# Optimization experiments

Hardware: AMD Instinct MI355X
Metric: run time of the kernel (lower is better)

## Reference

```python
import jax, jax.numpy as jnp
import numpy as np

B, L, NC, D = 4, 2048, 4096, 128
ITERS = 4
NHEAD = 8
T = L // 2
C2 = 2 * D


def _ln(x, g, b, eps=1e-5):
    m = jnp.mean(x, axis=-1, keepdims=True)
    v = jnp.var(x, axis=-1, keepdims=True)
    return (x - m) * jax.lax.rsqrt(v + eps) * g + b


def _mlp3(x, W1, b1, W2, b2, W3, b3):
    h = jax.nn.relu(x @ W1 + b1)
    h = jax.nn.relu(h @ W2 + b2)
    return h @ W3 + b3


def _lstm(inp, h, c, Wih, Whh, gi, bi, gh, bh, gc, bc):
    gates = _ln(inp @ Wih, gi, bi) + _ln(h @ Whh, gh, bh)
    i, f, g, o = jnp.split(gates, 4, axis=-1)
    cy = _ln(jax.nn.sigmoid(f) * c + jax.nn.sigmoid(i) * jnp.tanh(g), gc, bc)
    hy = jax.nn.sigmoid(o) * jnp.tanh(cy)
    return hy, cy


def _flip(x):
    # flip matrix with full literal counts == permutation swapping pos/neg halves
    half = x.shape[1] // 2
    return jnp.concatenate([x[:, half:], x[:, :half]], axis=1)


def setup_inputs():
    key = jax.random.key(0)
    ks = iter(jax.random.split(key, 64))
    def xav(fi, fo):
        s = float(np.sqrt(6.0 / (fi + fo)))
        return jax.random.uniform(next(ks), (fi, fo), jnp.float32, -s, s)
    def rn(*shape):
        return jax.random.normal(next(ks), shape, jnp.float32)
    inp = {}
    inp['adjacency_matrices'] = (jax.random.uniform(next(ks), (B, L, NC)) < 0.03).astype(jnp.float32)
    inp['batch_lit_counts'] = jnp.full((B,), L, dtype=jnp.int32)
    inp['L_init'] = rn(1, D) / np.sqrt(D).astype(np.float32)
    inp['C_init'] = rn(1, D) / np.sqrt(D).astype(np.float32)
    for p in ('LC', 'CL'):
        for i in (1, 2, 3):
            inp[p + '_W' + str(i)] = xav(D, D)
            inp[p + '_b' + str(i)] = jnp.full((D,), 0.01, jnp.float32)
    for p, isz in (('Lu', 2 * D), ('Cu', D)):
        inp[p + '_Wih'] = rn(isz, 4 * D)  # torch uses raw randn for LSTM weights
        inp[p + '_Whh'] = rn(D, 4 * D)
        for ln, n in (('lni', 4 * D), ('lnh', 4 * D), ('lnc', D)):
            inp[p + '_' + ln + '_g'] = jnp.ones((n,), jnp.float32)
            inp[p + '_' + ln + '_b'] = jnp.zeros((n,), jnp.float32)
    for p in ('k', 'q', 'v'):
        inp['att_W' + p] = xav(C2, C2)
        inp['att_b' + p] = jnp.zeros((C2,), jnp.float32)
    for p in ('asn', 'vote'):
        inp[p + '_W1'] = xav(C2, D)
        inp[p + '_b1'] = jnp.full((D,), 0.01, jnp.float32)
        inp[p + '_W2'] = xav(D, 1)
        inp[p + '_b2'] = jnp.full((1,), 0.01, jnp.float32)
    return inp


def reference(adjacency_matrices, batch_lit_counts, L_init, C_init,
              LC_W1, LC_b1, LC_W2, LC_b2, LC_W3, LC_b3,
              CL_W1, CL_b1, CL_W2, CL_b2, CL_W3, CL_b3,
              Lu_Wih, Lu_Whh, Lu_lni_g, Lu_lni_b, Lu_lnh_g, Lu_lnh_b, Lu_lnc_g, Lu_lnc_b,
              Cu_Wih, Cu_Whh, Cu_lni_g, Cu_lni_b, Cu_lnh_g, Cu_lnh_b, Cu_lnc_g, Cu_lnc_b,
              att_Wk, att_bk, att_Wq, att_bq, att_Wv, att_bv,
              asn_W1, asn_b1, asn_W2, asn_b2, vote_W1, vote_b1, vote_W2, vote_b2):
    A = adjacency_matrices
    Bb, Ll, Cc = A.shape
    Lh = jnp.broadcast_to(L_init, (Bb, Ll, D))
    Lc = jnp.zeros_like(Lh)
    Ch = jnp.broadcast_to(C_init, (Bb, Cc, D))
    Cxc = jnp.zeros_like(Ch)
    for _ in range(ITERS):
        # literal -> clause messages (gather via A^T)
        LC = jnp.einsum('blc,bld->bcd', A, _mlp3(Lh, LC_W1, LC_b1, LC_W2, LC_b2, LC_W3, LC_b3))
        Ch, Cxc = _lstm(LC, Ch, Cxc, Cu_Wih, Cu_Whh, Cu_lni_g, Cu_lni_b, Cu_lnh_g, Cu_lnh_b, Cu_lnc_g, Cu_lnc_b)
        # clause -> literal messages (scatter via A)
        CL = jnp.einsum('blc,bcd->bld', A, _mlp3(Ch, CL_W1, CL_b1, CL_W2, CL_b2, CL_W3, CL_b3))
        Lh, Lc = _lstm(jnp.concatenate([CL, _flip(Lh)], axis=-1), Lh, Lc,
                       Lu_Wih, Lu_Whh, Lu_lni_g, Lu_lni_b, Lu_lnh_g, Lu_lnh_b, Lu_lnc_g, Lu_lnc_b)
    # readout [h_l ; h_{~l}], positive literals only
    read = jnp.concatenate([Lh, _flip(Lh)], axis=-1)[:, :T]  # [B,T,2D]
    half = batch_lit_counts // 2
    mask = (jnp.arange(T)[None, :] < half[:, None]).astype(read.dtype)  # [B,T]
    read = read * mask[:, :, None]
    hd = C2 // NHEAD
    def heads(x, W, b):
        return (x @ W + b).reshape(Bb, T, NHEAD, hd).transpose(0, 2, 1, 3)
    k = heads(read, att_Wk, att_bk)
    q = heads(read, att_Wq, att_bq)
    v = heads(read, att_Wv, att_bv)
    att = jnp.einsum('bhtd,bhsd->bhts', q, k) * (1.0 / np.sqrt(hd))
    sq = (mask[:, None, :, None] * mask[:, None, None, :]) > 0  # [B,1,T,T]
    att = jnp.where(sq, att, -jnp.inf)
    att = jax.nn.softmax(att, axis=-1)
    att = jnp.where(jnp.isnan(att), 0.0, att)
    y = jnp.einsum('bhts,bhsd->bhtd', att, v).transpose(0, 2, 1, 3).reshape(Bb, T, C2)
    def head_mlp(x, W1, b1, W2, b2):
        return jax.nn.sigmoid(jax.nn.relu(x @ W1 + b1) @ W2 + b2)[..., 0]
    assignments = head_mlp(y, asn_W1, asn_b1, asn_W2, asn_b2) * mask  # [B,T]
    vote_vals = head_mlp(y, vote_W1, vote_b1, vote_W2, vote_b2)
    votes = jnp.sum(vote_vals * mask, axis=1) / jnp.maximum(jnp.sum(mask, axis=1), 1.0)
    return votes, assignments
```

## Files before the change

### kernel.cpp

```cpp
#include <hip/hip_runtime.h>


#define B_    4
#define L_    2048
#define NC_   4096
#define D_    128
#define ITERS_ 4
#define NH_   8
#define T_    1024
#define C2_   256
#define HD_   32
#define BL_   (B_*L_)
#define BNC_  (B_*NC_)
#define QS_   768

typedef unsigned short u16;
typedef __attribute__((ext_vector_type(8))) short b16x8;
typedef __attribute__((ext_vector_type(4))) float f32x4;

static __device__ __forceinline__ float bf2f(u16 u){
  union{unsigned int i; float f;} x; x.i = ((unsigned int)u) << 16; return x.f;
}
static __device__ __forceinline__ u16 f2bf(float f){
  union{float f; unsigned int i;} x; x.f = f;
// ... 41 lines not shown

#define NPJ_ 16
struct PJobs { const void* src[NPJ_]; unsigned n[NPJ_], N[NPJ_], koff[NPJ_],
               ksb[NPJ_], dh[NPJ_], dl[NPJ_]; };

__global__ __launch_bounds__(256) void k_prep(PJobs pj, u16* __restrict__ up,
                                              const int* __restrict__ flag){
  int jj = blockIdx.y;
  unsigned n = pj.n[jj];
  unsigned g = blockIdx.x*256 + threadIdx.x;
  if (g >= n) return;
  unsigned j = g & 7, lane = (g>>3)&63;
  unsigned ksb = pj.ksb[jj];
  unsigned ks = (g>>9) & ((1u<<ksb)-1u);
  unsigned nt = g >> (9+ksb);
  unsigned ncol = nt*16 + (lane&15);
  unsigned k = pj.koff[jj] + ks*32 + ((lane>>4)&3)*8 + j;
  unsigned si = k*pj.N[jj] + ncol;
  float v;
  if (*flag) v = bf2f(((const u16*)pj.src[jj])[si]);
  else       v = ((const float*)pj.src[jj])[si];
  u16 h,l; split2(v, h, l);
  up[pj.dh[jj] + g] = h;
  up[pj.dl[jj] + g] = l;
}

__global__ __launch_bounds__(256) void k_init(float* __restrict__ h, float* __restrict__ c,
                                              const float* __restrict__ init, int n){
  int i = blockIdx.x*256 + threadIdx.x;
  if (i < n){ h[i] = init[i & (D_-1)]; c[i] = 0.f; }
}

__global__ void k_zero_u(unsigned* __restrict__ p, int n){
  int i = blockIdx.x*256 + threadIdx.x; if (i < n) p[i] = 0u;
}
__global__ void k_zero(float* p, int n){
  int i = blockIdx.x*64 + threadIdx.x; if (i < n) p[i] = 0.f;
}

__global__ __launch_bounds__(128) void k_pack(const void* __restrict__ A,
    unsigned* __restrict__ bits, unsigned* __restrict__ cnt_l,
    const int* __restrict__ flag){
  const int row = blockIdx.x, w = threadIdx.x;
  unsigned m = 0;
  if (*flag){
    const ushort4* p = (const ushort4*)A + (size_t)row*(NC_/4) + w*8;
    #pragma unroll
    for (int i = 0; i < 8; i++){
      ushort4 u = p[i];
      m |= (unsigned)(u.x != 0) << (i*4);
      m |= (unsigned)(u.y != 0) << (i*4+1);
      m |= (unsigned)(u.z != 0) << (i*4+2);
      m |= (unsigned)(u.w != 0) << (i*4+3);
    }
  } else {
    const float4* p = (const float4*)A + (size_t)row*(NC_/4) + w*8;
    #pragma unroll
    for (int i = 0; i < 8; i++){
      float4 v = p[i];
      m |= (unsigned)(v.x != 0.f) << (i*4);
      m |= (unsigned)(v.y != 0.f) << (i*4+1);
      m |= (unsigned)(v.z != 0.f) << (i*4+2);
      m |= (unsigned)(v.w != 0.f) << (i*4+3);
    }
  }
  bits[(size_t)row*128 + w] = m;
  unsigned pc = __popc(m);
  #pragma unroll
  for (int o = 1; o < 64; o <<= 1) pc += __shfl_xor(pc, o);
  __shared__ unsigned ss[2];
  if ((w & 63) == 0) ss[w >> 6] = pc;
  __syncthreads();
  if (w == 0) cnt_l[row] = ss[0] + ss[1];
}

__global__ __launch_bounds__(256) void k_scan(unsigned* __restrict__ cnt,
    unsigned* __restrict__ off, int n){
  __shared__ unsigned ps[257];
  int t = threadIdx.x;
  int seg = n >> 8;
  int base = t*seg;
  unsigned s = 0;
  for (int i = 0; i < seg; i++) s += cnt[base+i];
  ps[t] = s;
  __syncthreads();
  if (t == 0){
    unsigned run = 0;
    for (int i = 0; i < 256; i++){ unsigned x = ps[i]; ps[i] = run; run += x; }
    ps[256] = run;
  }
  __syncthreads();
  unsigned run = ps[t];
  for (int i = 0; i < seg; i++){ off[base+i] = run; run += cnt[base+i]; cnt[base+i] = 0u; }
  if (t == 0) off[n] = ps[256];
}

__global__ __launch_bounds__(128) void k_fill_l(const unsigned* __restrict__ bits,
    const unsigned* __restrict__ off_l, u16* __restrict__ val_l,
    unsigned* __restrict__ cnt_c){
  const int row = blockIdx.x, w = threadIdx.x;
  const int b = row >> 11;
  unsigned m = bits[(size_t)row*128 + w];
  unsigned pc = __popc(m);
  __shared__ unsigned s[128];
  s[w] = pc; __syncthreads();
  #pragma unroll
  for (int o = 1; o < 128; o <<= 1){
    unsigned v = (w >= o) ? s[w-o] : 0u;
    __syncthreads();
    s[w] += v;
    __syncthreads();
  }
  unsigned base = off_l[row] + s[w] - pc;
  unsigned cb = ((unsigned)b << 12) + w*32;
  while (m){
    int j = __ffs(m) - 1; m &= m - 1;
    val_l[base++] = (u16)(w*32 + j);
    atomicAdd(cnt_c + cb + j, 1u);
  }
}

__global__ __launch_bounds__(256) void k_fill_c(const unsigned* __restrict__ bits,
    const unsigned* __restrict__ off_c, unsigned* __restrict__ cur_c,
    u16* __restrict__ val_c){
  int g = blockIdx.x*256 + threadIdx.x;
  unsigned m = bits[g];
  int row = g >> 7, w = g & 127;
  int b = row >> 11, l = row & (L_-1);
  unsigned cb = ((unsigned)b << 12) + w*32;
  while (m){
    int j = __ffs(m) - 1; m &= m - 1;
    unsigned idx = cb + j;
    unsigned pos = atomicAdd(cur_c + idx, 1u);
    val_c[off_c[idx] + pos] = (u16)l;
  }
}

__global__ __launch_bounds__(256) void k_spmm(const unsigned* __restrict__ off,
    const u16* __restrict__ val, const float* __restrict__ M, float* __restrict__ out,
    int sh1, int sh2){
  int row  = blockIdx.x*4 + (threadIdx.x >> 6);
  int lane = threadIdx.x & 63;
  unsigned p0 = off[row], p1 = off[row+1];
  const float2* Mp = (const float2*)M + (((size_t)(row >> sh1) << sh2) * 64) + lane;
  float x = 0.f, y = 0.f;
  for (unsigned p = p0; p < p1; ++p){
    float2 v = Mp[(size_t)val[p] * 64];
    x += v.x; y += v.y;
  }
  float2 r; r.x = x; r.y = y;
  ((float2*)out)[(size_t)row*64 + lane] = r;
}

__global__ __launch_bounds__(512) void k_mlp3m(const float* __restrict__ X,
    const u16* __restrict__ W1h, const u16* __restrict__ W1l,
    const u16* __restrict__ W2h, const u16* __restrict__ W2l,
    const u16* __restrict__ W3h, const u16* __restrict__ W3l,
    const float* __restrict__ b1, const float* __restrict__ b2,
    const float* __restrict__ b3, float* __restrict__ Y)
{
  __shared__ __align__(16) u16 Ah[32*136];
  __shared__ __align__(16) u16 Al[32*136];
  const int tid = threadIdx.x, lane = tid & 63, wv = tid >> 6;
  const int quad = lane >> 4, l15 = lane & 15;
  const int r0 = blockIdx.x * 32;
  {
    int row = tid >> 4, c0 = (tid & 15)*8;
    const float4* src = (const float4*)(X + (size_t)(r0+row)*128 + c0);
    float4 v0 = src[0], v1 = src[1];
    u16 h,l;
    split2(v0.x,h,l); Ah[row*136+c0]  =h; Al[row*136+c0]  =l;
    split2(v0.y,h,l); Ah[row*136+c0+1]=h; Al[row*136+c0+1]=l;
    split2(v0.z,h,l); Ah[row*136+c0+2]=h; Al[row*136+c0+2]=l;
    split2(v0.w,h,l); Ah[row*136+c0+3]=h; Al[row*136+c0+3]=l;
    split2(v1.x,h,l); Ah[row*136+c0+4]=h; Al[row*136+c0+4]=l;
    split2(v1.y,h,l); Ah[row*136+c0+5]=h; Al[row*136+c0+5]=l;
    split2(v1.z,h,l); Ah[row*136+c0+6]=h; Al[row*136+c0+6]=l;
    split2(v1.w,h,l); Ah[row*136+c0+7]=h; Al[row*136+c0+7]=l;
  }
  __syncthreads();
  const u16* Whs[3] = {W1h, W2h, W3h};
  const u16* Wls[3] = {W1l, W2l, W3l};
  const float* bs[3] = {b1, b2, b3};
  #pragma unroll
  for (int layer = 0; layer < 3; layer++){
    f32x4 acc[2] = {};
    #pragma unroll
    for (int ks = 0; ks < 4; ks++){
      b16x8 a_h[2], a_l[2];
      #pragma unroll
      for (int mt = 0; mt < 2; mt++){
        int ao = (mt*16 + l15)*136 + ks*32 + quad*8;
        a_h[mt] = *(const b16x8*)(Ah + ao);
        a_l[mt] = *(const b16x8*)(Al + ao);
      }
      size_t bo = (size_t)((wv*4 + ks)*64 + lane)*8;
      b16x8 bh = *(const b16x8*)(Whs[layer] + bo);
      b16x8 bl = *(const b16x8*)(Wls[layer] + bo);
      #pragma unroll
      for (int mt = 0; mt < 2; mt++){
        acc[mt] = __builtin_amdgcn_mfma_f32_16x16x32_bf16(a_h[mt], bh, acc[mt],0,0,0);
        acc[mt] = __builtin_amdgcn_mfma_f32_16x16x32_bf16(a_h[mt], bl, acc[mt],0,0,0);
        acc[mt] = __builtin_amdgcn_mfma_f32_16x16x32_bf16(a_l[mt], bh, acc[mt],0,0,0);
      }
    }
    int col = wv*16 + l15;
    if (layer < 2){
      float bb = bs[layer][col];
      __syncthreads();
      #pragma unroll
      for (int mt = 0; mt < 2; mt++)
        #pragma unroll
        for (int r = 0; r < 4; r++){
          int row = mt*16 + quad*4 + r;
          float v = fmaxf(acc[mt][r] + bb, 0.f);
          u16 h,l; split2(v,h,l);
          Ah[row*136 + col] = h; Al[row*136 + col] = l;
        }
      __syncthreads();
    } else {
      float bb = bs[2][col];
      #pragma unroll
      for (int mt = 0; mt < 2; mt++)
        #pragma unroll
        for (int r = 0; r < 4; r++){
          int row = mt*16 + quad*4 + r;
          Y[(size_t)(r0+row)*128 + col] = acc[mt][r] + bb;
        }
    }
  }
}

template<int NSEG>
__global__ __launch_bounds__(512) void k_lstm_mfma(
    const float* __restrict__ A0, const float* __restrict__ A1, const float* __restrict__ A2,
    int flip1,
    const u16* __restrict__ W0h, const u16* __restrict__ W0l,
    const u16* __restrict__ W1h, const u16* __restrict__ W1l,
    const u16* __restrict__ W2h, const u16* __restrict__ W2l,
    const float* __restrict__ lni_g, const float* __restrict__ lni_b,
    const float* __restrict__ lnh_g, const float* __restrict__ lnh_b,
    const float* __restrict__ lnc_g, const float* __restrict__ lnc_b,
    const float* __restrict__ c_in, float* __restrict__ c_out,
    float* __restrict__ h_out)
{
  __shared__ __align__(16) float G[32*516];
  __shared__ float red[8][32][4];
  __shared__ float st[32][4];
  u16* Ah = (u16*)G;
  u16* Al = Ah + 32*136;
  const int tid = threadIdx.x, lane = tid & 63, wv = tid >> 6;
  const int quad = lane >> 4, l15 = lane & 15;
  const int r0 = blockIdx.x * 32;

  f32x4 acc1[2][4] = {}, acc2[2][4] = {};

  #pragma unroll
  for (int s = 0; s < NSEG; ++s){
    const float* Ap = (s==0) ? A0 : ((s==1) ? A1 : A2);
    const u16* Wh = (s==0) ? W0h : ((s==1) ? W1h : W2h);
    const u16* Wl = (s==0) ? W0l : ((s==1) ? W1l : W2l);
    const int fm = (s==1) ? flip1 : 0;
    __syncthreads();
    {
      int row = tid >> 4, c0 = (tid & 15)*8;
      int arow = (r0 + row) ^ fm;
      const float4* src = (const float4*)(Ap + (size_t)arow*128 + c0);
      float4 v0 = src[0], v1 = src[1];
      u16 h,l;
      split2(v0.x,h,l); Ah[row*136+c0]  =h; Al[row*136+c0]  =l;
      split2(v0.y,h,l); Ah[row*136+c0+1]=h; Al[row*136+c0+1]=l;
      split2(v0.z,h,l); Ah[row*136+c0+2]=h; Al[row*136+c0+2]=l;
      split2(v0.w,h,l); Ah[row*136+c0+3]=h; Al[row*136+c0+3]=l;
      split2(v1.x,h,l); Ah[row*136+c0+4]=h; Al[row*136+c0+4]=l;
      split2(v1.y,h,l); Ah[row*136+c0+5]=h; Al[row*136+c0+5]=l;
      split2(v1.z,h,l); Ah[row*136+c0+6]=h; Al[row*136+c0+6]=l;
      split2(v1.w,h,l); Ah[row*136+c0+7]=h; Al[row*136+c0+7]=l;
    }
    __syncthreads();
    f32x4 (*accp)[4] = (s == NSEG-1) ? acc2 : acc1;
    #pragma unroll
    for (int ks = 0; ks < 4; ks++){
      b16x8 a_h[2], a_l[2];
      #pragma unroll
      for (int mt = 0; mt < 2; mt++){
        int ao = (mt*16 + l15)*136 + ks*32 + quad*8;
        a_h[mt] = *(const b16x8*)(Ah + ao);
        a_l[mt] = *(const b16x8*)(Al + ao);
      }
      #pragma unroll
      for (int ntl = 0; ntl < 4; ntl++){
        int nt = wv*4 + ntl;
        size_t bo = (size_t)((nt*4 + ks)*64 + lane)*8;
        b16x8 bh = *(const b16x8*)(Wh + bo);
        b16x8 bl = *(const b16x8*)(Wl + bo);
        #pragma unroll
        for (int mt = 0; mt < 2; mt++){
          accp[mt][ntl] = __builtin_amdgcn_mfma_f32_16x16x32_bf16(a_h[mt], bh, accp[mt][ntl],0,0,0);
          accp[mt][ntl] = __builtin_amdgcn_mfma_f32_16x16x32_bf16(a_h[mt], bl, accp[mt][ntl],0,0,0);
          accp[mt][ntl] = __builtin_amdgcn_mfma_f32_16x16x32_bf16(a_l[mt], bh, accp[mt][ntl],0,0,0);
        }
      }
    }
  }

  #pragma unroll
  for (int mt = 0; mt < 2; mt++)
    #pragma unroll
    for (int r = 0; r < 4; r++){
      float s1=0.f, q1=0.f, s2=0.f, q2=0.f;
      #pragma unroll
      for (int ntl = 0; ntl < 4; ntl++){
        float v1 = acc1[mt][ntl][r]; s1 += v1; q1 += v1*v1;
        float v2 = acc2[mt][ntl][r]; s2 += v2; q2 += v2*v2;
      }
      #pragma unroll
      for (int m = 1; m < 16; m <<= 1){
        s1 += __shfl_xor(s1, m); q1 += __shfl_xor(q1, m);
        s2 += __shfl_xor(s2, m); q2 += __shfl_xor(q2, m);
      }
      if (l15 == 0){
        int row = mt*16 + quad*4 + r;
        red[wv][row][0]=s1; red[wv][row][1]=q1; red[wv][row][2]=s2; red[wv][row][3]=q2;
      }
    }
  __syncthreads();
  if (tid < 32){
    int row = tid;
    float s1=0.f,q1=0.f,s2=0.f,q2=0.f;
    #pragma unroll
    for (int w = 0; w < 8; w++){
      s1 += red[w][row][0]; q1 += red[w][row][1];
      s2 += red[w][row][2]; q2 += red[w][row][3];
    }
    const float i512 = 1.f/512.f;
    float m1 = s1*i512, v1 = fmaxf(q1*i512 - m1*m1, 0.f);
    float m2 = s2*i512, v2 = fmaxf(q2*i512 - m2*m2, 0.f);
    st[row][0] = m1; st[row][1] = rsqrtf(v1 + 1e-5f);
    st[row][2] = m2; st[row][3] = rsqrtf(v2 + 1e-5f);
  }
  __syncthreads();

  #pragma unroll
  for (int mt = 0; mt < 2; mt++)
    #pragma unroll
    for (int ntl = 0; ntl < 4; ntl++){
      int col = wv*64 + ntl*16 + l15;
      float gi = lni_g[col], bi = lni_b[col];
      float gh = lnh_g[col], bh = lnh_b[col];
      #pragma unroll
      for (int r = 0; r < 4; r++){
        int row = mt*16 + quad*4 + r;
        float v = (acc1[mt][ntl][r] - st[row][0])*st[row][1]*gi + bi
                + (acc2[mt][ntl][r] - st[row][2])*st[row][3]*gh + bh;
        G[row*516 + col] = v;
      }
    }
  __syncthreads();

  float lcg0 = lnc_g[lane], lcb0 = lnc_b[lane];
  float lcg1 = lnc_g[lane+64], lcb1 = lnc_b[lane+64];
  const float i128 = 1.f/128.f;
  #pragma unroll
  for (int i = 0; i < 4; i++){
    int row = wv*4 + i;
    int rg = r0 + row;
    float cp[2], sc = 0.f, qc = 0.f;
    #pragma unroll
    for (int jj = 0; jj < 2; jj++){
      int c = lane + 64*jj;
      float iv = sigm(G[row*516 + c]);
      float fv = sigm(G[row*516 + 128 + c]);
      float gv = tanhf(G[row*516 + 256 + c]);
      cp[jj] = fv * c_in[(size_t)rg*128 + c] + iv*gv;
      sc += cp[jj]; qc += cp[jj]*cp[jj];
    }
    #pragma unroll
    for (int m = 1; m < 64; m <<= 1){ sc += __shfl_xor(sc, m); qc += __shfl_xor(qc, m); }
    float mc = sc*i128, vc = fmaxf(qc*i128 - mc*mc, 0.f), rsc = rsqrtf(vc + 1e-5f);
    #pragma unroll
    for (int jj = 0; jj < 2; jj++){
      int c = lane + 64*jj;
      float cy = (cp[jj]-mc)*rsc*(jj ? lcg1 : lcg0) + (jj ? lcb1 : lcb0);
      c_out[(size_t)rg*128 + c] = cy;
      float ov = sigm(G[row*516 + 384 + c]);
      h_out[(size_t)rg*128 + c] = ov*tanhf(cy);
    }
  }
}

template<int NT, int NSPLIT, int KK32, int ACT, int GATHER>
__global__ __launch_bounds__(512) void k_gemm_mfma(const float* __restrict__ A,
    const u16* __restrict__ Wh, const u16* __restrict__ Wl,
    const float* __restrict__ bias, float* __restrict__ Y,
    const int* __restrict__ counts)
{
  const int NTOT = NSPLIT*8*NT*16;
  const int LDA = KK32*32 + 8;
  __shared__ __align__(16) u16 Ah[32*(KK32*32+8)];
  __shared__ __align__(16) u16 Al[32*(KK32*32+8)];
  const int tid = threadIdx.x, lane = tid & 63, wv = tid >> 6;
  const int quad = lane >> 4, l15 = lane & 15;
  const int r0 = blockIdx.x * 32, by = blockIdx.y;
  {
    int row = tid >> 4, c0 = (tid & 15)*(KK32*2);
    if (GATHER){
      int r = r0 + row; int b = r >> 10; int t = r & 1023;
      int half = counts[b] / 2; if (half > T_) half = T_;
      float msk = (t < half) ? 1.f : 0.f;
      #pragma unroll
      for (int q4 = 0; q4 < KK32/2; q4++){
        int c = c0 + q4*4;
        const float* src = A + ((size_t)(b*L_ + t + ((c >= 128) ? T_ : 0))*128 + (c & 127));
        float4 v = *(const float4*)src;
        u16 h,l;
        split2(v.x*msk,h,l); Ah[row*LDA+c]  =h; Al[row*LDA+c]  =l;
        split2(v.y*msk,h,l); Ah[row*LDA+c+1]=h; Al[row*LDA+c+1]=l;
        split2(v.z*msk,h,l); Ah[row*LDA+c+2]=h; Al[row*LDA+c+2]=l;
        split2(v.w*msk,h,l); Ah[row*LDA+c+3]=h; Al[row*LDA+c+3]=l;
      }
    } else {
      const float4* src = (const float4*)(A + (size_t)(r0+row)*(KK32*32) + c0);
      #pragma unroll
      for (int q4 = 0; q4 < KK32/2; q4++){
        float4 v = src[q4]; int c = c0 + q4*4;
        u16 h,l;
        split2(v.x,h,l); Ah[row*LDA+c]  =h; Al[row*LDA+c]  =l;
        split2(v.y,h,l); Ah[row*LDA+c+1]=h; Al[row*LDA+c+1]=l;
        split2(v.z,h,l); Ah[row*LDA+c+2]=h; Al[row*LDA+c+2]=l;
        split2(v.w,h,l); Ah[row*LDA+c+3]=h; Al[row*LDA+c+3]=l;
      }
    }
  }
  __syncthreads();
  f32x4 acc[2][NT] = {};
  #pragma unroll
  for (int ks = 0; ks < KK32; ks++){
    b16x8 a_h[2], a_l[2];
    #pragma unroll
    for (int mt = 0; mt < 2; mt++){
      int ao = (mt*16 + l15)*LDA + ks*32 + quad*8;
      a_h[mt] = *(const b16x8*)(Ah + ao);
      a_l[mt] = *(const b16x8*)(Al + ao);
    }
    #pragma unroll
    for (int ntl = 0; ntl < NT; ntl++){
      int nt = by*(8*NT) + wv*NT + ntl;
      size_t bo = (size_t)((nt*KK32 + ks)*64 + lane)*8;
      b16x8 bh = *(const b16x8*)(Wh + bo);
      b16x8 bl = *(const b16x8*)(Wl + bo);
      #pragma unroll
      for (int mt = 0; mt < 2; mt++){
        acc[mt][ntl] = __builtin_amdgcn_mfma_f32_16x16x32_bf16(a_h[mt], bh, acc[mt][ntl],0,0,0);
        acc[mt][ntl] = __builtin_amdgcn_mfma_f32_16x16x32_bf16(a_h[mt], bl, acc[mt][ntl],0,0,0);
        acc[mt][ntl] = __builtin_amdgcn_mfma_f32_16x16x32_bf16(a_l[mt], bh, acc[mt][ntl],0,0,0);
      }
    }
  }
  #pragma unroll
  for (int mt = 0; mt < 2; mt++)
    #pragma unroll
    for (int ntl = 0; ntl < NT; ntl++){
      int colg = by*(8*NT*16) + wv*(NT*16) + ntl*16 + l15;
      float bb = bias[colg];
      #pragma unroll
      for (int r = 0; r < 4; r++){
        int row = mt*16 + quad*4 + r;
        float v = acc[mt][ntl][r] + bb;
        if (ACT) v = fmaxf(v, 0.f);
        Y[(size_t)(r0+row)*NTOT + colg] = v;
      }
    }
}

__global__ __launch_bounds__(256) void k_attn_split(const float* __restrict__ qkv,
    const int* __restrict__ counts, float* __restrict__ Pa, float* __restrict__ ML)
{
  const int z = blockIdx.z, b = z >> 1, part = z & 1;
  const int h = blockIdx.y, t0 = blockIdx.x*64;
  int half = counts[b] / 2; if (half > T_) half = T_; if (half < 0) half = 0;
  const int sbeg = part*512;
  const int send = (half < sbeg + 512) ? half : (sbeg + 512);
  if (t0 >= half || sbeg >= send) return;
  const int tid = threadIdx.x;
  const int lane = tid & 63, wv = tid >> 6;
  const int lr = tid >> 2, lc = (tid & 3)*8;

  __shared__ float Qs[64][36];
  __shared__ float Ks[64][32];
  __shared__ float Ss[64][68];

  {
    const float* qp = qkv + (size_t)(b*T_ + t0 + lr)*QS_ + h*HD_ + lc;
    float4 a0 = *(const float4*)qp;
    float4 a1 = *(const float4*)(qp+4);
    *(float4*)&Qs[lr][lc]   = a0;
    *(float4*)&Qs[lr][lc+4] = a1;
  }

  const int ty = tid >> 4, tx = tid & 15;
  const int sr = wv*16 + (lane & 15);
  const int spart = (lane >> 4) * 16;
  const int rp = lane >> 3, cq = lane & 7;
  const int r0 = wv*16 + rp*2;

  float4 acc0 = {0.f,0.f,0.f,0.f}, acc1 = {0.f,0.f,0.f,0.f};
  float mst = -3e38f, lst = 0.f;
  const float scale = 0.17677669529663687f;
  const int ntile = (send - sbeg + 63) >> 6;

  for (int st = 0; st < ntile; ++st){
    const int s0 = sbeg + st*64;
    __syncthreads();
    {
      const float* kp = qkv + (size_t)(b*T_ + s0 + lr)*QS_ + 256 + h*HD_ + lc;
      float4 k0 = *(const float4*)kp;
      float4 k1 = *(const float4*)(kp+4);
      int key = (lr >> 2) & 7;
      int c0 = lc >> 2;
      *(float4*)&Ks[lr][4*((c0  ) ^ key)] = k0;
      *(float4*)&Ks[lr][4*((c0+1) ^ key)] = k1;
    }
    __syncthreads();

    float s4[4][4];
    #pragma unroll
    for (int i = 0; i < 4; i++)
      #pragma unroll
      for (int j = 0; j < 4; j++) s4[i][j] = 0.f;
    const int xk = tx & 7;
    #pragma unroll
    for (int kk4 = 0; kk4 < 8; kk4++){
      float4 a4[4], b4[4];
      #pragma unroll
      for (int i = 0; i < 4; i++) a4[i] = *(const float4*)&Qs[ty*4+i][kk4*4];
      const int pk = 4*(kk4 ^ xk);
      #pragma unroll
      for (int j = 0; j < 4; j++) b4[j] = *(const float4*)&Ks[tx*4+j][pk];
      #pragma unroll
      for (int i = 0; i < 4; i++)
        #pragma unroll
        for (int j = 0; j < 4; j++)
          s4[i][j] += a4[i].x*b4[j].x + a4[i].y*b4[j].y + a4[i].z*b4[j].z + a4[i].w*b4[j].w;
    }
    #pragma unroll
    for (int i = 0; i < 4; i++){
      float4 w4;
      w4.x = (s0 + tx*4 + 0 < half) ? s4[i][0]*scale : -1e30f;
      w4.y = (s0 + tx*4 + 1 < half) ? s4[i][1]*scale : -1e30f;
      w4.z = (s0 + tx*4 + 2 < half) ? s4[i][2]*scale : -1e30f;
      w4.w = (s0 + tx*4 + 3 < half) ? s4[i][3]*scale : -1e30f;
      *(float4*)&Ss[ty*4+i][tx*4] = w4;
    }

    float pvv[16];
    float vmax = -3e38f;
    #pragma unroll
    for (int c4 = 0; c4 < 4; c4++){
      float4 t4 = *(const float4*)&Ss[sr][spart + c4*4];
      pvv[c4*4+0] = t4.x; pvv[c4*4+1] = t4.y; pvv[c4*4+2] = t4.z; pvv[c4*4+3] = t4.w;
      vmax = fmaxf(vmax, fmaxf(fmaxf(t4.x, t4.y), fmaxf(t4.z, t4.w)));
    }
    vmax = fmaxf(vmax, __shfl_xor(vmax, 16));
    vmax = fmaxf(vmax, __shfl_xor(vmax, 32));
    float nm = fmaxf(mst, vmax);
    float alpha = expf(mst - nm);
    float psum = 0.f;
    #pragma unroll
    for (int c = 0; c < 16; c++){
      float p = expf(pvv[c] - nm);
      pvv[c] = p; psum += p;
    }
    psum += __shfl_xor(psum, 16);
    psum += __shfl_xor(psum, 32);
    lst = lst*alpha + psum;
    mst = nm;
    #pragma unroll
    for (int c4 = 0; c4 < 4; c4++){
      float4 w4; w4.x = pvv[c4*4+0]; w4.y = pvv[c4*4+1]; w4.z = pvv[c4*4+2]; w4.w = pvv[c4*4+3];
      *(float4*)&Ss[sr][spart + c4*4] = w4;
    }
    float al0 = __shfl(alpha, 2*rp);
    float al1 = __shfl(alpha, 2*rp + 1);
    acc0.x *= al0; acc0.y *= al0; acc0.z *= al0; acc0.w *= al0;
    acc1.x *= al1; acc1.y *= al1; acc1.z *= al1; acc1.w *= al1;

    const float* vbase = qkv + (size_t)(b*T_ + s0)*QS_ + 512 + h*HD_ + cq*4;
    #pragma unroll 4
    for (int kk4 = 0; kk4 < 16; kk4++){
      float4 p0 = *(const float4*)&Ss[r0  ][kk4*4];
      float4 p1 = *(const float4*)&Ss[r0+1][kk4*4];
      float4 v0 = *(const float4*)(vbase + (size_t)(kk4*4+0)*QS_);
      float4 v1 = *(const float4*)(vbase + (size_t)(kk4*4+1)*QS_);
      float4 v2 = *(const float4*)(vbase + (size_t)(kk4*4+2)*QS_);
      float4 v3 = *(const float4*)(vbase + (size_t)(kk4*4+3)*QS_);
      acc0.x += p0.x*v0.x + p0.y*v1.x + p0.z*v2.x + p0.w*v3.x;
      acc0.y += p0.x*v0.y + p0.y*v1.y + p0.z*v2.y + p0.w*v3.y;
      acc0.z += p0.x*v0.z + p0.y*v1.z + p0.z*v2.z + p0.w*v3.z;
      acc0.w += p0.x*v0.w + p0.y*v1.w + p0.z*v2.w + p0.w*v3.w;
      acc1.x += p1.x*v0.x + p1.y*v1.x + p1.z*v2.x + p1.w*v3.x;
      acc1.y += p1.x*v0.y + p1.y*v1.y + p1.z*v2.y + p1.w*v3.y;
      acc1.z += p1.x*v0.z + p1.y*v1.z + p1.z*v2.z + p1.w*v3.z;
      acc1.w += p1.x*v0.w + p1.y*v1.w + p1.z*v2.w + p1.w*v3.w;
    }
  }

  const int prow0 = (b*NH_ + h)*T_ + t0;
  float* accP = Pa + (size_t)part*1048576;
  *(float4*)(accP + (size_t)(prow0 + r0    )*32 + cq*4) = acc0;
  *(float4*)(accP + (size_t)(prow0 + r0 + 1)*32 + cq*4) = acc1;
  if (lane < 16){
    float* mlP = ML + (size_t)part*65536;
    int rr = prow0 + wv*16 + lane;
    mlP[(size_t)rr*2]   = mst;
    mlP[(size_t)rr*2+1] = lst;
  }
}

__global__ __launch_bounds__(256) void k_attn_comb(const float* __restrict__ Pa,
    const float* __restrict__ ML, const int* __restrict__ counts,
    float* __restrict__ y)
{
  int g = blockIdx.x*256 + threadIdx.x;
  int r = g >> 8, c = g & 255;
  int b = r >> 10, t = r & 1023;
  int h = c >> 5, cc = c & 31;
  int half = counts[b] / 2; if (half > T_) half = T_;
  float out = 0.f;
  if (t < half){
    int prow = (b*NH_ + h)*T_ + t;
    float m0 = ML[(size_t)prow*2], l0 = ML[(size_t)prow*2+1];
    float a0 = Pa[(size_t)prow*32 + cc];
    if (half > 512){
      float m1 = ML[65536 + (size_t)prow*2], l1 = ML[65536 + (size_t)prow*2+1];
      float a1 = Pa[1048576 + (size_t)prow*32 + cc];
      float m = fmaxf(m0, m1);
      float w0 = expf(m0 - m), w1 = expf(m1 - m);
      float den = w0*l0 + w1*l1;
      out = (den > 0.f) ? (w0*a0 + w1*a1)/den : 0.f;
    } else {
      out = (l0 > 0.f) ? a0/l0 : 0.f;
    }
  }
  y[(size_t)r*256 + c] = out;
}

__global__ __launch_bounds__(128) void k_final(const float* __restrict__ hv,
    const float* __restrict__ aW2, const float* __restrict__ ab2,
    const float* __restrict__ vW2, const float* __restrict__ vb2,
    const int* __restrict__ counts, void* __restrict__ outv,
    float* __restrict__ vote_sum, const int* __restrict__ flag)
{
  int row = blockIdx.x, tid = threadIdx.x;
  int b = row / T_, t = row - b*T_;
  int half = counts[b] / 2; if (half > T_) half = T_;
  float pa = hv[(size_t)row*256 + tid]       * aW2[tid];
  float pv = hv[(size_t)row*256 + 128 + tid] * vW2[tid];
  #pragma unroll
  for (int off = 32; off > 0; off >>= 1){ pa += __shfl_down(pa, off); pv += __shfl_down(pv, off); }
  __shared__ float r[2][2];
  int wid = tid >> 6, lane = tid & 63;
  if (lane == 0){ r[0][wid] = pa; r[1][wid] = pv; }
  __syncthreads();
  if (tid == 0){
    float a  = sigm(r[0][0] + r[0][1] + ab2[0]);
    float vv = sigm(r[1][0] + r[1][1] + vb2[0]);
    bool mk = (t < half);
    float av = mk ? a : 0.f;
    if (*flag) ((u16*)outv)[4 + row] = f2bf(av);
    else       ((float*)outv)[4 + row] = av;
    if (mk) atomicAdd(vote_sum + b, vv);
  }
}

__global__ void k_votes(const float* __restrict__ vote_sum, const int* __restrict__ counts,
                        void* __restrict__ outv, const int* __restrict__ flag){
  int b = threadIdx.x;
  if (b < B_){
    int half = counts[b] / 2; if (half > T_) half = T_;
    float den = (float)(half > 1 ? half : 1);
    float vv = vote_sum[b] / den;
    if (*flag) ((u16*)outv)[b] = f2bf(vv);
    else       ((float*)outv)[b] = vv;
  }
}

extern "C" void kernel_launch(void* const* d_in, const int* in_sizes, int n_in,
                              void* d_out, int out_size, void* d_ws, size_t ws_size,
                              hipStream_t stream)
{
  const void* A_adj = d_in[0];
  const int* counts = (const int*)d_in[1];

  const size_t M1 = (size_t)1048576;
  const size_t NEED = (5*M1 + M1 + 2*M1 + 2*M1 + 700416 + 16416 + 8224
                       + 16384 + 8192 + 520000 + 520000 + 32) * sizeof(float);
  if (ws_size < NEED) return;

  float* ws = (float*)d_ws;
  float* R    = ws;
  float* Lc   = R + 5*M1;
  float* Ch   = Lc + M1;
  float* Cc   = Ch + 2*M1;
  float* wp   = Cc + 2*M1;
  unsigned* off_c = (unsigned*)(wp + 700416);
  unsigned* off_l = off_c + 16416;
  unsigned* cnt_c = off_l + 8224;
  unsigned* cnt_l = cnt_c + 16384;
  u16* val_c = (u16*)(cnt_l + 8192);
  u16* val_l = (u16*)((float*)val_c + 520000);
  float* tail = (float*)val_l + 520000;
  float* vote_sum = tail;
  int* flag = (int*)(tail + 8);
  unsigned* bits = (unsigned*)R;

  float* R0 = R, *R1 = R + M1, *R2 = R + 2*M1, *R3 = R + 3*M1, *R4 = R + 4*M1;

  k_detect<<<1, 256, 0, stream>>>((const unsigned int*)A_adj, flag);

  CJobs cj;
  int ncj = 0;
  unsigned off = 0;
  auto cadd = [&](int idx, unsigned n)->float*{
    cj.src[ncj] = d_in[idx]; cj.n[ncj] = n; cj.off[ncj] = off;
    float* p = wp + off; off += (n + 3u) & ~3u; ncj++; return p;
  };
  float* Linit = cadd(2, 128);
  float* Cinit = cadd(3, 128);
  float *LC_b1 = cadd(5, 128), *LC_b2 = cadd(7, 128), *LC_b3 = cadd(9, 128);
  float *CL_b1 = cadd(11,128), *CL_b2 = cadd(13,128), *CL_b3 = cadd(15,128);
  float *Lu_lni_g = cadd(18,512), *Lu_lni_b = cadd(19,512);
  float *Lu_lnh_g = cadd(20,512), *Lu_lnh_b = cadd(21,512);
  float *Lu_lnc_g = cadd(22,128), *Lu_lnc_b = cadd(23,128);
  float *Cu_lni_g = cadd(26,512), *Cu_lni_b = cadd(27,512);
  float *Cu_lnh_g = cadd(28,512), *Cu_lnh_b = cadd(29,512);
  float *Cu_lnc_g = cadd(30,128), *Cu_lnc_b = cadd(31,128);
  float *asn_W2 = cadd(40,128), *asn_b2 = cadd(41,1);
  float *vote_W2 = cadd(44,128), *vote_b2 = cadd(45,1);
  float* bqkv = wp + off;
  cj.src[ncj]=d_in[35]; cj.n[ncj]=256; cj.off[ncj]=off;       ncj++;
  cj.src[ncj]=d_in[33]; cj.n[ncj]=256; cj.off[ncj]=off+256;   ncj++;
  cj.src[ncj]=d_in[37]; cj.n[ncj]=256; cj.off[ncj]=off+512;   ncj++;
  off += 768;
  float* bhv = wp + off;
  cj.src[ncj]=d_in[39]; cj.n[ncj]=128; cj.off[ncj]=off;       ncj++;
  cj.src[ncj]=d_in[43]; cj.n[ncj]=128; cj.off[ncj]=off+128;   ncj++;
  off += 256;
  { dim3 g(2, NCJ_); k_cvt_all<<<g, 256, 0, stream>>>(cj, wp, flag); }

  u16* up = (u16*)(wp + ((off + 3u) & ~3u));
  PJobs pj;
  int npj = 0;
  unsigned uoff = 0;
  auto padd = [&](int idx, unsigned n, unsigned Nw, unsigned koff, unsigned ksb,
                  unsigned dsth, unsigned dstl){
    pj.src[npj]=d_in[idx]; pj.n[npj]=n; pj.N[npj]=Nw; pj.koff[npj]=koff;
    pj.ksb[npj]=ksb; pj.dh[npj]=dsth; pj.dl[npj]=dstl; npj++;
  };
  auto solo = [&](int idx, unsigned n, unsigned Nw, unsigned koff, unsigned ksb,
                  const u16** h, const u16** l){
    padd(idx, n, Nw, koff, ksb, uoff, uoff + n);
    *h = up + uoff; *l = up + uoff + n; uoff += 2*n;
  };
  const u16 *lc1h,*lc1l,*lc2h,*lc2l,*lc3h,*lc3l,*cl1h,*cl1l,*cl2h,*cl2l,*cl3h,*cl3l;
  const u16 *cwih_h,*cwih_l,*cwhh_h,*cwhh_l;
  const u16 *lwa_h,*lwa_l,*lwb_h,*lwb_l,*lwhh_h,*lwhh_l;
  solo(4, 16384,128,0,2,&lc1h,&lc1l);  solo(6, 16384,128,0,2,&lc2h,&lc2l);
  solo(8, 16384,128,0,2,&lc3h,&lc3l);  solo(10,16384,128,0,2,&cl1h,&cl1l);
  solo(12,16384,128,0,2,&cl2h,&cl2l);  solo(14,16384,128,0,2,&cl3h,&cl3l);
  solo(24,65536,512,0,2,&cwih_h,&cwih_l);
  solo(25,65536,512,0,2,&cwhh_h,&cwhh_l);
  solo(16,65536,512,0,  2,&lwa_h,&lwa_l);
  solo(16,65536,512,128,2,&lwb_h,&lwb_l);
  solo(17,65536,512,0,2,&lwhh_h,&lwhh_l);
  const u16* wqkv_h = up + uoff;
  const u16* wqkv_l = up + uoff + 196608;
  padd(34, 65536, 256, 0, 3, uoff,           uoff+196608);
  padd(32, 65536, 256, 0, 3, uoff+65536,     uoff+196608+65536);
  padd(36, 65536, 256, 0, 3, uoff+131072,    uoff+196608+131072);
  uoff += 393216;
  const u16* whv_h = up + uoff;
  const u16* whv_l = up + uoff + 65536;
  padd(38, 32768, 128, 0, 3, uoff,        uoff+65536);
  padd(42, 32768, 128, 0, 3, uoff+32768,  uoff+65536+32768);
  uoff += 131072;
  { dim3 g(256, NPJ_); k_prep<<<g, 256, 0, stream>>>(pj, up, flag); }

  k_zero_u<<<(16384+255)/256, 256, 0, stream>>>(cnt_c, 16384);
  k_pack<<<BL_, 128, 0, stream>>>(A_adj, bits, cnt_l, flag);
  k_scan<<<1, 256, 0, stream>>>(cnt_l, off_l, 8192);
  k_fill_l<<<BL_, 128, 0, stream>>>(bits, off_l, val_l, cnt_c);
  k_scan<<<1, 256, 0, stream>>>(cnt_c, off_c, 16384);
  k_fill_c<<<4096, 256, 0, stream>>>(bits, off_c, cnt_c, val_c);

  k_init<<<(BL_*D_)/256, 256, 0, stream>>>(R0, Lc, Linit, BL_*D_);
  k_init<<<(BNC_*D_)/256, 256, 0, stream>>>(Ch, Cc, Cinit, BNC_*D_);

  for (int it = 0; it < ITERS_; ++it){
    bool ev = ((it & 1) == 0);
    float* cur  = ev ? R0 : R4;
    float* msgL = ev ? R1 : R0;
    float* LCb  = ev ? R2 : R1;
    float* msgC = LCb;
    float* CLb  = ev ? R1 : R3;
    float* nxt  = ev ? R4 : R0;

    k_mlp3m<<<BL_/32, 512, 0, stream>>>(cur, lc1h,lc1l, lc2h,lc2l, lc3h,lc3l,
                                        LC_b1, LC_b2, LC_b3, msgL);
    k_spmm<<<BNC_/4, 256, 0, stream>>>(off_c, val_c, msgL, LCb, 12, 11);
    k_lstm_mfma<2><<<BNC_/32, 512, 0, stream>>>(LCb, Ch, nullptr, 0,
        cwih_h, cwih_l, cwhh_h, cwhh_l, nullptr, nullptr,
        Cu_lni_g, Cu_lni_b, Cu_lnh_g, Cu_lnh_b, Cu_lnc_g, Cu_lnc_b, Cc, Cc, Ch);
    k_mlp3m<<<BNC_/32, 512, 0, stream>>>(Ch, cl1h,cl1l, cl2h,cl2l, cl3h,cl3l,
                                         CL_b1, CL_b2, CL_b3, msgC);
    k_spmm<<<BL_/4, 256, 0, stream>>>(off_l, val_l, msgC, CLb, 11, 12);
    k_lstm_mfma<3><<<BL_/32, 512, 0, stream>>>(CLb, cur, cur, 1024,
        lwa_h, lwa_l, lwb_h, lwb_l, lwhh_h, lwhh_l,
        Lu_lni_g, Lu_lni_b, Lu_lnh_g, Lu_lnh_b, Lu_lnc_g, Lu_lnc_b, Lc, Lc, nxt);
  }
  float* Lh = R0;

  float* qkvb  = Ch;
  float* yb    = R1;
  float* hv    = R2;

  { dim3 g((B_*T_)/32, 2);
    k_gemm_mfma<3,2,8,0,1><<<g, 512, 0, stream>>>(Lh, wqkv_h, wqkv_l, bqkv, qkvb, counts); }
  { dim3 g(T_/64, NH_, B_*2);
    k_attn_split<<<g, 256, 0, stream>>>(qkvb, counts, R3, Lc); }
  k_attn_comb<<<4096, 256, 0, stream>>>(R3, Lc, counts, yb);
  { dim3 g((B_*T_)/32, 2);
    k_gemm_mfma<1,2,8,1,0><<<g, 512, 0, stream>>>(yb, whv_h, whv_l, bhv, hv, counts); }
  k_zero<<<1, 64, 0, stream>>>(vote_sum, B_);
  k_final<<<B_*T_, 128, 0, stream>>>(hv, asn_W2, asn_b2, vote_W2, vote_b2,
                                     counts, d_out, vote_sum, flag);
  k_votes<<<1, 64, 0, stream>>>(vote_sum, counts, d_out, flag);
}
```

Baseline: 1.692 ms.

## Shrink MFMA GEMM row tiles to 16 rows with 256-thread blocks

The MLP, LSTM and generic GEMM kernels move from 32-row tiles with 8 waves to 16-row tiles with 4 waves. Each wave now covers twice as many output column tiles from a single A fragment, and the grids double in size. Launch bounds now request 4 blocks per CU, which may raise occupancy and shrink LDS per block. The cost is that each weight fragment is reused across only one row tile, so global weight traffic per row doubles, and register pressure per wave rises. The attention PV loop unroll is also lowered.

```diff
diff --git a/kernel.cpp b/kernel.cpp
--- a/kernel.cpp
+++ b/kernel.cpp
@@ -217,18 +217,18 @@
   ((float2*)out)[(size_t)row*64 + lane] = r;
 }
 
-__global__ __launch_bounds__(512) void k_mlp3m(const float* __restrict__ X,
+__global__ __launch_bounds__(256, 4) void k_mlp3m(const float* __restrict__ X,
     const u16* __restrict__ W1h, const u16* __restrict__ W1l,
     const u16* __restrict__ W2h, const u16* __restrict__ W2l,
     const u16* __restrict__ W3h, const u16* __restrict__ W3l,
     const float* __restrict__ b1, const float* __restrict__ b2,
     const float* __restrict__ b3, float* __restrict__ Y)
 {
-  __shared__ __align__(16) u16 Ah[32*136];
-  __shared__ __align__(16) u16 Al[32*136];
+  __shared__ __align__(16) u16 Ah[16*136];
+  __shared__ __align__(16) u16 Al[16*136];
   const int tid = threadIdx.x, lane = tid & 63, wv = tid >> 6;
   const int quad = lane >> 4, l15 = lane & 15;
-  const int r0 = blockIdx.x * 32;
+  const int r0 = blockIdx.x * 16;
   {
     int row = tid >> 4, c0 = (tid & 15)*8;
     const float4* src = (const float4*)(X + (size_t)(r0+row)*128 + c0);
@@ -252,52 +252,52 @@
     f32x4 acc[2] = {};
     #pragma unroll
     for (int ks = 0; ks < 4; ks++){
-      b16x8 a_h[2], a_l[2];
-      #pragma unroll
-      for (int mt = 0; mt < 2; mt++){
-        int ao = (mt*16 + l15)*136 + ks*32 + quad*8;
-        a_h[mt] = *(const b16x8*)(Ah + ao);
-        a_l[mt] = *(const b16x8*)(Al + ao);
+      int ao = l15*136 + ks*32 + quad*8;
+      b16x8 a_h = *(const b16x8*)(Ah + ao);
+      b16x8 a_l = *(const b16x8*)(Al + ao);
+      #pragma unroll
+      for (int ntl = 0; ntl < 2; ntl++){
+        int nt = wv*2 + ntl;
+        size_t bo = (size_t)((nt*4 + ks)*64 + lane)*8;
+        b16x8 bh = *(const b16x8*)(Whs[layer] + bo);
+        b16x8 bl = *(const b16x8*)(Wls[layer] + bo);
+        acc[ntl] = __builtin_amdgcn_mfma_f32_16x16x32_bf16(a_h, bh, acc[ntl],0,0,0);
+        acc[ntl] = __builtin_amdgcn_mfma_f32_16x16x32_bf16(a_h, bl, acc[ntl],0,0,0);
+        acc[ntl] = __builtin_amdgcn_mfma_f32_16x16x32_bf16(a_l, bh, acc[ntl],0,0,0);
       }
-      size_t bo = (size_t)((wv*4 + ks)*64 + lane)*8;
-      b16x8 bh = *(const b16x8*)(Whs[layer] + bo);
-      b16x8 bl = *(const b16x8*)(Wls[layer] + bo);
-      #pragma unroll
-      for (int mt = 0; mt < 2; mt++){
-        acc[mt] = __builtin_amdgcn_mfma_f32_16x16x32_bf16(a_h[mt], bh, acc[mt],0,0,0);
-        acc[mt] = __builtin_amdgcn_mfma_f32_16x16x32_bf16(a_h[mt], bl, acc[mt],0,0,0);
-        acc[mt] = __builtin_amdgcn_mfma_f32_16x16x32_bf16(a_l[mt], bh, acc[mt],0,0,0);
-      }
-    }
-    int col = wv*16 + l15;
+    }
     if (layer < 2){
-      float bb = bs[layer][col];
       __syncthreads();
       #pragma unroll
-      for (int mt = 0; mt < 2; mt++)
+      for (int ntl = 0; ntl < 2; ntl++){
+        int col = wv*32 + ntl*16 + l15;
+        float bb = bs[layer][col];
         #pragma unroll
         for (int r = 0; r < 4; r++){
-          int row = mt*16 + quad*4 + r;
-          float v = fmaxf(acc[mt][r] + bb, 0.f);
+          int row = quad*4 + r;
+          float v = fmaxf(acc[ntl][r] + bb, 0.f);
           u16 h,l; split2(v,h,l);
           Ah[row*136 + col] = h; Al[row*136 + col] = l;
         }
+      }
       __syncthreads();
     } else {
-      float bb = bs[2][col];
-      #pragma unroll
-      for (int mt = 0; mt < 2; mt++)
+      #pragma unroll
+      for (int ntl = 0; ntl < 2; ntl++){
+        int col = wv*32 + ntl*16 + l15;
+        float bb = bs[2][col];
         #pragma unroll
         for (int r = 0; r < 4; r++){
-          int row = mt*16 + quad*4 + r;
-          Y[(size_t)(r0+row)*128 + col] = acc[mt][r] + bb;
+          int row = quad*4 + r;
+          Y[(size_t)(r0+row)*128 + col] = acc[ntl][r] + bb;
         }
+      }
     }
   }
 }
 
 template<int NSEG>
-__global__ __launch_bounds__(512) void k_lstm_mfma(
+__global__ __launch_bounds__(256, 4) void k_lstm_mfma(
     const float* __restrict__ A0, const float* __restrict__ A1, const float* __restrict__ A2,
     int flip1,
     const u16* __restrict__ W0h, const u16* __restrict__ W0l,
@@ -309,16 +309,16 @@
     const float* __restrict__ c_in, float* __restrict__ c_out,
     float* __restrict__ h_out)
 {
-  __shared__ __align__(16) float G[32*516];
-  __shared__ float red[8][32][4];
-  __shared__ float st[32][4];
+  __shared__ __align__(16) float G[16*516];
+  __shared__ float red[4][16][4];
+  __shared__ float st[16][4];
   u16* Ah = (u16*)G;
-  u16* Al = Ah + 32*136;
+  u16* Al = Ah + 16*136;
   const int tid = threadIdx.x, lane = tid & 63, wv = tid >> 6;
   const int quad = lane >> 4, l15 = lane & 15;
-  const int r0 = blockIdx.x * 32;
-
-  f32x4 acc1[2][4] = {}, acc2[2][4] = {};
+  const int r0 = blockIdx.x * 16;
+
+  f32x4 acc1[8] = {}, acc2[8] = {};
 
   #pragma unroll
   for (int s = 0; s < NSEG; ++s){
@@ -343,58 +343,49 @@
       split2(v1.w,h,l); Ah[row*136+c0+7]=h; Al[row*136+c0+7]=l;
     }
     __syncthreads();
-    f32x4 (*accp)[4] = (s == NSEG-1) ? acc2 : acc1;
+    f32x4 (*accp) = (s == NSEG-1) ? acc2 : acc1;
     #pragma unroll
     for (int ks = 0; ks < 4; ks++){
-      b16x8 a_h[2], a_l[2];
-      #pragma unroll
-      for (int mt = 0; mt < 2; mt++){
-        int ao = (mt*16 + l15)*136 + ks*32 + quad*8;
-        a_h[mt] = *(const b16x8*)(Ah + ao);
-        a_l[mt] = *(const b16x8*)(Al + ao);
-      }
-      #pragma unroll
-      for (int ntl = 0; ntl < 4; ntl++){
-        int nt = wv*4 + ntl;
+      int ao = l15*136 + ks*32 + quad*8;
+      b16x8 a_h = *(const b16x8*)(Ah + ao);
+      b16x8 a_l = *(const b16x8*)(Al + ao);
+      #pragma unroll
+      for (int ntl = 0; ntl < 8; ntl++){
+        int nt = wv*8 + ntl;
         size_t bo = (size_t)((nt*4 + ks)*64 + lane)*8;
         b16x8 bh = *(const b16x8*)(Wh + bo);
         b16x8 bl = *(const b16x8*)(Wl + bo);
-        #pragma unroll
-        for (int mt = 0; mt < 2; mt++){
-          accp[mt][ntl] = __builtin_amdgcn_mfma_f32_16x16x32_bf16(a_h[mt], bh, accp[mt][ntl],0,0,0);
-          accp[mt][ntl] = __builtin_amdgcn_mfma_f32_16x16x32_bf16(a_h[mt], bl, accp[mt][ntl],0,0,0);
-          accp[mt][ntl] = __builtin_amdgcn_mfma_f32_16x16x32_bf16(a_l[mt], bh, accp[mt][ntl],0,0,0);
-        }
+        accp[ntl] = __builtin_amdgcn_mfma_f32_16x16x32_bf16(a_h, bh, accp[ntl],0,0,0);
+        accp[ntl] = __builtin_amdgcn_mfma_f32_16x16x32_bf16(a_h, bl, accp[ntl],0,0,0);
+        accp[ntl] = __builtin_amdgcn_mfma_f32_16x16x32_bf16(a_l, bh, accp[ntl],0,0,0);
       }
     }
   }
 
   #pragma unroll
-  for (int mt = 0; mt < 2; mt++)
-    #pragma unroll
-    for (int r = 0; r < 4; r++){
-      float s1=0.f, q1=0.f, s2=0.f, q2=0.f;
-      #pragma unroll
-      for (int ntl = 0; ntl < 4; ntl++){
-        float v1 = acc1[mt][ntl][r]; s1 += v1; q1 += v1*v1;
-        float v2 = acc2[mt][ntl][r]; s2 += v2; q2 += v2*v2;
-      }
-      #pragma unroll
-      for (int m = 1; m < 16; m <<= 1){
-        s1 += __shfl_xor(s1, m); q1 += __shfl_xor(q1, m);
-        s2 += __shfl_xor(s2, m); q2 += __shfl_xor(q2, m);
-      }
-      if (l15 == 0){
-        int row = mt*16 + quad*4 + r;
-        red[wv][row][0]=s1; red[wv][row][1]=q1; red[wv][row][2]=s2; red[wv][row][3]=q2;
-      }
-    }
+  for (int r = 0; r < 4; r++){
+    float s1=0.f, q1=0.f, s2=0.f, q2=0.f;
+    #pragma unroll
+    for (int ntl = 0; ntl < 8; ntl++){
+      float v1 = acc1[ntl][r]; s1 += v1; q1 += v1*v1;
+      float v2 = acc2[ntl][r]; s2 += v2; q2 += v2*v2;
+    }
+    #pragma unroll
+    for (int m = 1; m < 16; m <<= 1){
+      s1 += __shfl_xor(s1, m); q1 += __shfl_xor(q1, m);
+      s2 += __shfl_xor(s2, m); q2 += __shfl_xor(q2, m);
+    }
+    if (l15 == 0){
+      int row = quad*4 + r;
+      red[wv][row][0]=s1; red[wv][row][1]=q1; red[wv][row][2]=s2; red[wv][row][3]=q2;
+    }
+  }
   __syncthreads();
-  if (tid < 32){
+  if (tid < 16){
     int row = tid;
     float s1=0.f,q1=0.f,s2=0.f,q2=0.f;
     #pragma unroll
-    for (int w = 0; w < 8; w++){
+    for (int w = 0; w < 4; w++){
       s1 += red[w][row][0]; q1 += red[w][row][1];
       s2 += red[w][row][2]; q2 += red[w][row][3];
     }
@@ -407,20 +398,18 @@
   __syncthreads();
 
   #pragma unroll
-  for (int mt = 0; mt < 2; mt++)
-    #pragma unroll
-    for (int ntl = 0; ntl < 4; ntl++){
-      int col = wv*64 + ntl*16 + l15;
-      float gi = lni_g[col], bi = lni_b[col];
-      float gh = lnh_g[col], bh = lnh_b[col];
-      #pragma unroll
-      for (int r = 0; r < 4; r++){
-        int row = mt*16 + quad*4 + r;
-        float v = (acc1[mt][ntl][r] - st[row][0])*st[row][1]*gi + bi
-                + (acc2[mt][ntl][r] - st[row][2])*st[row][3]*gh + bh;
-        G[row*516 + col] = v;
-      }
-    }
+  for (int ntl = 0; ntl < 8; ntl++){
+    int col = wv*128 + ntl*16 + l15;
+    float gi = lni_g[col], bi = lni_b[col];
+    float gh = lnh_g[col], bh = lnh_b[col];
+    #pragma unroll
+    for (int r = 0; r < 4; r++){
+      int row = quad*4 + r;
+      float v = (acc1[ntl][r] - st[row][0])*st[row][1]*gi + bi
+              + (acc2[ntl][r] - st[row][2])*st[row][3]*gh + bh;
+      G[row*516 + col] = v;
+    }
+  }
   __syncthreads();
 
   float lcg0 = lnc_g[lane], lcb0 = lnc_b[lane];
@@ -455,18 +444,18 @@
 }
 
 template<int NT, int NSPLIT, int KK32, int ACT, int GATHER>
-__global__ __launch_bounds__(512) void k_gemm_mfma(const float* __restrict__ A,
+__global__ __launch_bounds__(256, 4) void k_gemm_mfma(const float* __restrict__ A,
     const u16* __restrict__ Wh, const u16* __restrict__ Wl,
     const float* __restrict__ bias, float* __restrict__ Y,
     const int* __restrict__ counts)
 {
-  const int NTOT = NSPLIT*8*NT*16;
+  const int NTOT = NSPLIT*4*NT*16;
   const int LDA = KK32*32 + 8;
-  __shared__ __align__(16) u16 Ah[32*(KK32*32+8)];
-  __shared__ __align__(16) u16 Al[32*(KK32*32+8)];
+  __shared__ __align__(16) u16 Ah[16*(KK32*32+8)];
+  __shared__ __align__(16) u16 Al[16*(KK32*32+8)];
   const int tid = threadIdx.x, lane = tid & 63, wv = tid >> 6;
   const int quad = lane >> 4, l15 = lane & 15;
-  const int r0 = blockIdx.x * 32, by = blockIdx.y;
+  const int r0 = blockIdx.x * 16, by = blockIdx.y;
   {
     int row = tid >> 4, c0 = (tid & 15)*(KK32*2);
     if (GATHER){
@@ -498,47 +487,38 @@
     }
   }
   __syncthreads();
-  f32x4 acc[2][NT] = {};
+  f32x4 acc[NT] = {};
   #pragma unroll
   for (int ks = 0; ks < KK32; ks++){
-    b16x8 a_h[2], a_l[2];
-    #pragma unroll
-    for (int mt = 0; mt < 2; mt++){
-      int ao = (mt*16 + l15)*LDA + ks*32 + quad*8;
-      a_h[mt] = *(const b16x8*)(Ah + ao);
-      a_l[mt] = *(const b16x8*)(Al + ao);
-    }
+    int ao = l15*LDA + ks*32 + quad*8;
+    b16x8 a_h = *(const b16x8*)(Ah + ao);
+    b16x8 a_l = *(const b16x8*)(Al + ao);
     #pragma unroll
     for (int ntl = 0; ntl < NT; ntl++){
-      int nt = by*(8*NT) + wv*NT + ntl;
+      int nt = by*(4*NT) + wv*NT + ntl;
       size_t bo = (size_t)((nt*KK32 + ks)*64 + lane)*8;
       b16x8 bh = *(const b16x8*)(Wh + bo);
       b16x8 bl = *(const b16x8*)(Wl + bo);
-      #pragma unroll
-      for (int mt = 0; mt < 2; mt++){
-        acc[mt][ntl] = __builtin_amdgcn_mfma_f32_16x16x32_bf16(a_h[mt], bh, acc[mt][ntl],0,0,0);
-        acc[mt][ntl] = __builtin_amdgcn_mfma_f32_16x16x32_bf16(a_h[mt], bl, acc[mt][ntl],0,0,0);
-        acc[mt][ntl] = __builtin_amdgcn_mfma_f32_16x16x32_bf16(a_l[mt], bh, acc[mt][ntl],0,0,0);
-      }
-    }
-  }
-  #pragma unroll
-  for (int mt = 0; mt < 2; mt++)
-    #pragma unroll
-    for (int ntl = 0; ntl < NT; ntl++){
-      int colg = by*(8*NT*16) + wv*(NT*16) + ntl*16 + l15;
-      float bb = bias[colg];
-      #pragma unroll
-      for (int r = 0; r < 4; r++){
-        int row = mt*16 + quad*4 + r;
-        float v = acc[mt][ntl][r] + bb;
-        if (ACT) v = fmaxf(v, 0.f);
-        Y[(size_t)(r0+row)*NTOT + colg] = v;
-      }
-    }
-}
-
-__global__ __launch_bounds__(256) void k_attn_split(const float* __restrict__ qkv,
+      acc[ntl] = __builtin_amdgcn_mfma_f32_16x16x32_bf16(a_h, bh, acc[ntl],0,0,0);
+      acc[ntl] = __builtin_amdgcn_mfma_f32_16x16x32_bf16(a_h, bl, acc[ntl],0,0,0);
+      acc[ntl] = __builtin_amdgcn_mfma_f32_16x16x32_bf16(a_l, bh, acc[ntl],0,0,0);
+    }
+  }
+  #pragma unroll
+  for (int ntl = 0; ntl < NT; ntl++){
+    int colg = by*(4*NT*16) + wv*(NT*16) + ntl*16 + l15;
+    float bb = bias[colg];
+    #pragma unroll
+    for (int r = 0; r < 4; r++){
+      int row = quad*4 + r;
+      float v = acc[ntl][r] + bb;
+      if (ACT) v = fmaxf(v, 0.f);
+      Y[(size_t)(r0+row)*NTOT + colg] = v;
+    }
+  }
+}
+
+__global__ __launch_bounds__(256, 4) void k_attn_split(const float* __restrict__ qkv,
     const int* __restrict__ counts, float* __restrict__ Pa, float* __restrict__ ML)
 {
   const int z = blockIdx.z, b = z >> 1, part = z & 1;
@@ -651,7 +631,7 @@
     acc1.x *= al1; acc1.y *= al1; acc1.z *= al1; acc1.w *= al1;
 
     const float* vbase = qkv + (size_t)(b*T_ + s0)*QS_ + 512 + h*HD_ + cq*4;
-    #pragma unroll 4
+    #pragma unroll 2
     for (int kk4 = 0; kk4 < 16; kk4++){
       float4 p0 = *(const float4*)&Ss[r0  ][kk4*4];
       float4 p1 = *(const float4*)&Ss[r0+1][kk4*4];
@@ -870,16 +850,16 @@
     float* CLb  = ev ? R1 : R3;
     float* nxt  = ev ? R4 : R0;
 
-    k_mlp3m<<<BL_/32, 512, 0, stream>>>(cur, lc1h,lc1l, lc2h,lc2l, lc3h,lc3l,
+    k_mlp3m<<<BL_/16, 256, 0, stream>>>(cur, lc1h,lc1l, lc2h,lc2l, lc3h,lc3l,
                                         LC_b1, LC_b2, LC_b3, msgL);
     k_spmm<<<BNC_/4, 256, 0, stream>>>(off_c, val_c, msgL, LCb, 12, 11);
-    k_lstm_mfma<2><<<BNC_/32, 512, 0, stream>>>(LCb, Ch, nullptr, 0,
+    k_lstm_mfma<2><<<BNC_/16, 256, 0, stream>>>(LCb, Ch, nullptr, 0,
         cwih_h, cwih_l, cwhh_h, cwhh_l, nullptr, nullptr,
         Cu_lni_g, Cu_lni_b, Cu_lnh_g, Cu_lnh_b, Cu_lnc_g, Cu_lnc_b, Cc, Cc, Ch);
-    k_mlp3m<<<BNC_/32, 512, 0, stream>>>(Ch, cl1h,cl1l, cl2h,cl2l, cl3h,cl3l,
+    k_mlp3m<<<BNC_/16, 256, 0, stream>>>(Ch, cl1h,cl1l, cl2h,cl2l, cl3h,cl3l,
                                          CL_b1, CL_b2, CL_b3, msgC);
     k_spmm<<<BL_/4, 256, 0, stream>>>(off_l, val_l, msgC, CLb, 11, 12);
-    k_lstm_mfma<3><<<BL_/32, 512, 0, stream>>>(CLb, cur, cur, 1024,
+    k_lstm_mfma<3><<<BL_/16, 256, 0, stream>>>(CLb, cur, cur, 1024,
         lwa_h, lwa_l, lwb_h, lwb_l, lwhh_h, lwhh_l,
         Lu_lni_g, Lu_lni_b, Lu_lnh_g, Lu_lnh_b, Lu_lnc_g, Lu_lnc_b, Lc, Lc, nxt);
   }
@@ -889,13 +869,13 @@
   float* yb    = R1;
   float* hv    = R2;
 
-  { dim3 g((B_*T_)/32, 2);
-    k_gemm_mfma<3,2,8,0,1><<<g, 512, 0, stream>>>(Lh, wqkv_h, wqkv_l, bqkv, qkvb, counts); }
+  { dim3 g((B_*T_)/16, 2);
+    k_gemm_mfma<6,2,8,0,1><<<g, 256, 0, stream>>>(Lh, wqkv_h, wqkv_l, bqkv, qkvb, counts); }
   { dim3 g(T_/64, NH_, B_*2);
     k_attn_split<<<g, 256, 0, stream>>>(qkvb, counts, R3, Lc); }
   k_attn_comb<<<4096, 256, 0, stream>>>(R3, Lc, counts, yb);
-  { dim3 g((B_*T_)/32, 2);
-    k_gemm_mfma<1,2,8,1,0><<<g, 512, 0, stream>>>(yb, whv_h, whv_l, bhv, hv, counts); }
+  { dim3 g((B_*T_)/16, 2);
+    k_gemm_mfma<2,2,8,1,0><<<g, 256, 0, stream>>>(yb, whv_h, whv_l, bhv, hv, counts); }
   k_zero<<<1, 64, 0, stream>>>(vote_sum, B_);
   k_final<<<B_*T_, 128, 0, stream>>>(hv, asn_W2, asn_b2, vote_W2, vote_b2,
                                      counts, d_out, vote_sum, flag);
```

Result: slower. 2.783 ms (+64.4%).
